# Optimization experiments

Hardware: AMD Instinct MI355X
Metric: run time of the kernel (lower is better)

## Reference

```python
import jax, jax.numpy as jnp
import numpy as np

EMBED = 1024
HEADS = 16
GQA_GROUPS = 2
KV_HEADS = HEADS // GQA_GROUPS  # 8
HEAD_DIM = EMBED // HEADS       # 64
ALIBI_ALPHA = 1.0
START_I = 0
N, S = 2, 2048


def setup_inputs() -> dict:
    key = jax.random.key(0)
    ks = jax.random.split(key, 6)
    x = jax.random.normal(ks[0], (N, S, EMBED), dtype=jnp.float32)
    sc = 1.0 / np.sqrt(EMBED)
    Wq = jax.random.normal(ks[1], (HEADS * HEAD_DIM, EMBED), dtype=jnp.float32) * sc
    Wk = jax.random.normal(ks[2], (KV_HEADS * HEAD_DIM, EMBED), dtype=jnp.float32) * sc
    Wv = jax.random.normal(ks[3], (KV_HEADS * HEAD_DIM, EMBED), dtype=jnp.float32) * sc
    Wo = jax.random.normal(ks[4], (EMBED, HEADS * HEAD_DIM), dtype=jnp.float32) * sc
    bo = jax.random.normal(ks[5], (EMBED,), dtype=jnp.float32) * 0.01
    return {"x": x, "Wq": Wq, "Wk": Wk, "Wv": Wv, "Wo": Wo, "bo": bo}


def _alibi_bias(q_len, k_len):
    # slopes[i] = 2**(-alpha*(i+start)) for i in 1..heads  -> shape (1,H,1,1)
    i = jnp.arange(1, HEADS + 1, dtype=jnp.float32)
    slopes = jnp.exp2(-ALIBI_ALPHA * (i + START_I)).reshape(1, HEADS, 1, 1)
    t_q = jnp.arange(q_len, dtype=jnp.float32)
    t_k = jnp.arange(k_len, dtype=jnp.float32)
    dist = jnp.abs(t_q[:, None] - t_k[None, :])  # (Q,K), symmetric (non-causal ALiBi)
    return -dist[None, None] * slopes            # (1,H,Q,K)


def reference(x, Wq, Wk, Wv, Wo, bo):
    n, s, _ = x.shape
    q = (x @ Wq.T).reshape(n, s, HEADS, HEAD_DIM)      # nqhd
    k = (x @ Wk.T).reshape(n, s, KV_HEADS, HEAD_DIM)   # nkhd (kv heads)
    v = (x @ Wv.T).reshape(n, s, KV_HEADS, HEAD_DIM)
    # GQA: repeat_interleave kv heads along head dim
    k = jnp.repeat(k, GQA_GROUPS, axis=2)
    v = jnp.repeat(v, GQA_GROUPS, axis=2)
    energy = jnp.einsum("nqhd,nkhd->nhqk", q, k)
    energy = energy + _alibi_bias(s, s)
    # NOTE: original divides (energy + bias) by sqrt(head_dim) inside softmax
    attn = jax.nn.softmax(energy / jnp.sqrt(jnp.float32(HEAD_DIM)), axis=-1)
    out = jnp.einsum("nhqk,nkhd->nqhd", attn, v).reshape(n, s, HEADS * HEAD_DIM)
    return out @ Wo.T + bo
```

## Files before the change

kernel.cpp:

```cpp
#include <hip/hip_runtime.h>

typedef _Float16 f16;
typedef f16 f16x8 __attribute__((ext_vector_type(8)));
typedef f16 f16x4 __attribute__((ext_vector_type(4)));
typedef float f32x4 __attribute__((ext_vector_type(4)));
typedef float f32x16 __attribute__((ext_vector_type(16)));
typedef unsigned uint4v __attribute__((ext_vector_type(4)));

#define GLL(g, l) __builtin_amdgcn_global_load_lds((const __attribute__((address_space(1))) void*)(g), (__attribute__((address_space(3))) void*)(l), 16, 0, 0)

__global__ __launch_bounds__(256) void cvt_all(
    const float* __restrict__ x, const float* __restrict__ wq, const float* __restrict__ wk,
    const float* __restrict__ wv, const float* __restrict__ wo,
    f16* __restrict__ xh, f16* __restrict__ wqh, f16* __restrict__ wkh,
    f16* __restrict__ wvh, f16* __restrict__ woh)
{
  int i = blockIdx.x * 256 + threadIdx.x;
  const float4* src; f16x4* dst; int off;
  if (i < 1048576)      { src = (const float4*)x;  dst = (f16x4*)xh;  off = i; }
  else if (i < 1310720) { src = (const float4*)wq; dst = (f16x4*)wqh; off = i - 1048576; }
  else if (i < 1441792) { src = (const float4*)wk; dst = (f16x4*)wkh; off = i - 1310720; }
  else if (i < 1572864) { src = (const float4*)wv; dst = (f16x4*)wvh; off = i - 1441792; }
  else                  { src = (const float4*)wo; dst = (f16x4*)woh; off = i - 1572864; }
  float4 v = src[off];
  f16x4 hv; hv[0] = (f16)v.x; hv[1] = (f16)v.y; hv[2] = (f16)v.z; hv[3] = (f16)v.w;
  dst[off] = hv;
}

template<int MODE>
__global__ __launch_bounds__(256) void gemm_k(
    const f16* __restrict__ A, const f16* __restrict__ B0, const f16* __restrict__ B1,
    const f16* __restrict__ B2,
    f16* __restrict__ Qb, f16* __restrict__ Kb, f16* __restrict__ VTb,
    const float* __restrict__ bo, float* __restrict__ Co)
{
  __shared__ __align__(16) f16 Ah[2][4096];
  __shared__ __align__(16) f16 Bh[2][4096];
  const int tid = threadIdx.x;
  const int bm = blockIdx.x & 31, bn = blockIdx.x >> 5;
  const f16* Bp;
  if (MODE == 0) {
    if (bn < 8)       Bp = B0 + (size_t)bn * 131072;
    else if (bn < 12) Bp = B1 + (size_t)(bn - 8) * 131072;
    else              Bp = B2 + (size_t)(bn - 12) * 131072;
  } else {
    Bp = B0 + (size_t)bn * 131072;
  }
  const f16* Ap = A + (size_t)bm * 131072;

  const int w = tid >> 6, lane = tid & 63, lr = lane & 15, lg = lane >> 4;
  const int wr = w >> 1, wc = w & 1;

  auto stage = [&](int b, int kt) {
#pragma unroll
    for (int i = 0; i < 2; ++i) {
      int o = tid * 16 + i * 4096;
      int row = o >> 6, colb = o & 63;
      GLL((const char*)Ap + (size_t)row * 2048 + kt * 64 + colb, (char*)&Ah[b][0] + o);
      GLL((const char*)Bp + (size_t)row * 2048 + kt * 64 + colb, (char*)&Bh[b][0] + o);
    }
  };

  f32x4 acc[4][4] = {};

  stage(0, 0);
  for (int kt = 0; kt < 32; ++kt) {
    const int cur = kt & 1;
    __syncthreads();
    if (kt < 31) stage(cur ^ 1, kt + 1);
    f16x8 af[4], bf[4];
#pragma unroll
    for (int mi = 0; mi < 4; ++mi)
      af[mi] = *(const f16x8*)((const char*)&Ah[cur][0] + (wr * 64 + mi * 16 + lr) * 64 + lg * 16);
#pragma unroll
    for (int ni = 0; ni < 4; ++ni)
      bf[ni] = *(const f16x8*)((const char*)&Bh[cur][0] + (wc * 64 + ni * 16 + lr) * 64 + lg * 16);
#pragma unroll
    for (int mi = 0; mi < 4; ++mi)
#pragma unroll
      for (int ni = 0; ni < 4; ++ni)
        acc[mi][ni] = __builtin_amdgcn_mfma_f32_16x16x32_f16(af[mi], bf[ni], acc[mi][ni], 0, 0, 0);
    __syncthreads();
  }

#pragma unroll
  for (int mi = 0; mi < 4; ++mi) {
#pragma unroll
    for (int ni = 0; ni < 4; ++ni) {
      const int ncol = bn * 128 + wc * 64 + ni * 16 + lr;
#pragma unroll
      for (int j = 0; j < 4; ++j) {
        const int m = bm * 128 + wr * 64 + mi * 16 + lg * 4 + j;
        const float v = acc[mi][ni][j];
        if (MODE == 0) {
          const int nb = m >> 11, s = m & 2047;
          if (ncol < 1024) {
            const int hh = ncol >> 6, d = ncol & 63;
            Qb[(((size_t)(nb * 16 + hh)) * 2048 + s) * 64 + d] = (f16)v;
          } else if (ncol < 1536) {
            const int kh = (ncol - 1024) >> 6, d = ncol & 63;
            Kb[(((size_t)(nb * 8 + kh)) * 2048 + s) * 64 + d] = (f16)v;
          } else {
            const int vh = (ncol - 1536) >> 6, d = ncol & 63;
            VTb[(((size_t)(nb * 8 + vh)) * 64 + d) * 2048 + s] = (f16)v;
          }
        } else {
          Co[(size_t)m * 1024 + ncol] = v + bo[ncol];
        }
      }
    }
  }
}

__global__ __launch_bounds__(256, 2) void attn_k(
    const f16* __restrict__ Qb, const f16* __restrict__ Kb, const f16* __restrict__ VTb,
    f16* __restrict__ Ob)
{
  __shared__ __align__(16) f16 KV[2][2][4096];

  const int tid = threadIdx.x, w = tid >> 6, l = tid & 63;
  const int lq = l & 31, hi = l >> 5;
  const int qt = blockIdx.x, nh = blockIdx.y;
  const int n = nh >> 4, h = nh & 15, kvh = h >> 1;
  const int qb = qt * 128;
  const int qhat = qb + w * 32 + lq;

  const f16* Qp = Qb + ((size_t)(n * 16 + h) * 2048 + qhat) * 64;
  f16x8 qf[4];
#pragma unroll
  for (int cd = 0; cd < 4; ++cd)
    qf[cd] = *(const f16x8*)(Qp + cd * 16 + hi * 8);

  const char* Kg = (const char*)(Kb + (size_t)(n * 8 + kvh) * 2048 * 64);
  const char* Vg = (const char*)(VTb + (size_t)(n * 8 + kvh) * 64 * 2048);

  const int s0 = tid * 16, s1 = tid * 16 + 4096;
  const int r0 = s0 >> 7, c0 = ((s0 >> 4) & 7) ^ (r0 & 7);
  const int r1 = s1 >> 7, c1 = ((s1 >> 4) & 7) ^ (r1 & 7);

  auto stageK = [&](int buf, int tb) {
    GLL(Kg + (size_t)(tb * 64 + r0) * 128 + c0 * 16, (char*)&KV[buf][0][0] + s0);
    GLL(Kg + (size_t)(tb * 64 + r1) * 128 + c1 * 16, (char*)&KV[buf][0][0] + s1);
  };
  auto stageV = [&](int buf, int tb) {
    GLL(Vg + (size_t)r0 * 4096 + tb * 128 + c0 * 16, (char*)&KV[buf][1][0] + s0);
    GLL(Vg + (size_t)r1 * 4096 + tb * 128 + c1 * 16, (char*)&KV[buf][1][0] + s1);
  };

  f32x16 oacc[2] = {};
  float p[2][16];
  float m_r = -1e30f, l_r = 0.f;
  const float C1 = 0.18033688011112042f;
  const float slt = exp2f(-(float)(h + 1)) * C1;
  const float qpos = (float)qhat;

  stageK(0, 0); stageV(0, 0);

  for (int t = 0; t < 32; ++t) {
    const int cur = t & 1;
    __syncthreads();
    if (t < 31) { stageK(cur ^ 1, t + 1); stageV(cur ^ 1, t + 1); }

#pragma unroll
    for (int kt = 0; kt < 2; ++kt) {
      f32x16 c = {};
#pragma unroll
      for (int cd = 0; cd < 4; ++cd) {
        const int row = kt * 32 + lq;
        f16x8 kf = *(const f16x8*)((const char*)&KV[cur][0][0] + row * 128 + (((2 * cd + hi) ^ (row & 7)) * 16));
        c = __builtin_amdgcn_mfma_f32_32x32x16_f16(kf, qf[cd], c, 0, 0, 0);
      }
      const float kb0 = (float)(t * 64 + kt * 32 + 4 * hi);
#pragma unroll
      for (int r = 0; r < 16; ++r) {
        float kpos = kb0 + (float)((r & 3) + 8 * (r >> 2));
        p[kt][r] = c[r] * C1 - fabsf(qpos - kpos) * slt;
      }
    }
    float pmax = p[0][0];
#pragma unroll
    for (int kt = 0; kt < 2; ++kt)
#pragma unroll
      for (int r = 0; r < 16; ++r) pmax = fmaxf(pmax, p[kt][r]);
    pmax = fmaxf(pmax, __shfl_xor(pmax, 32));

    if (!__all(pmax - m_r <= 8.0f)) {
      float mn = fmaxf(m_r, pmax);
      float sc = __builtin_amdgcn_exp2f(m_r - mn);
      m_r = mn; l_r *= sc;
#pragma unroll
      for (int dt = 0; dt < 2; ++dt)
#pragma unroll
        for (int r = 0; r < 16; ++r) oacc[dt][r] *= sc;
    }
    float ps = 0.f;
#pragma unroll
    for (int kt = 0; kt < 2; ++kt)
#pragma unroll
      for (int r = 0; r < 16; ++r) {
        float e = __builtin_amdgcn_exp2f(p[kt][r] - m_r);
        p[kt][r] = e; ps += e;
      }
    ps += __shfl_xor(ps, 32);
    l_r += ps;

    f16x8 pf[4];
#pragma unroll
    for (int c2 = 0; c2 < 4; ++c2) {
      const int T = c2 >> 1, e = c2 & 1;
      unsigned w0 = __builtin_bit_cast(unsigned, __builtin_amdgcn_cvt_pkrtz(p[T][8 * e + 0], p[T][8 * e + 1]));
      unsigned w2 = __builtin_bit_cast(unsigned, __builtin_amdgcn_cvt_pkrtz(p[T][8 * e + 4], p[T][8 * e + 5]));
      unsigned w1 = __builtin_bit_cast(unsigned, __builtin_amdgcn_cvt_pkrtz(p[T][8 * e + 2], p[T][8 * e + 3]));
      unsigned w3 = __builtin_bit_cast(unsigned, __builtin_amdgcn_cvt_pkrtz(p[T][8 * e + 6], p[T][8 * e + 7]));
      asm volatile("v_permlane32_swap_b32 %0, %1" : "+v"(w0), "+v"(w2));
      asm volatile("v_permlane32_swap_b32 %0, %1" : "+v"(w1), "+v"(w3));
      uint4v pu; pu.x = w0; pu.y = w1; pu.z = w2; pu.w = w3;
      pf[c2] = __builtin_bit_cast(f16x8, pu);
    }

#pragma unroll
    for (int dt = 0; dt < 2; ++dt) {
#pragma unroll
      for (int ck = 0; ck < 4; ++ck) {
        const int row = dt * 32 + lq;
        f16x8 vf = *(const f16x8*)((const char*)&KV[cur][1][0] + row * 128 + (((2 * ck + hi) ^ (row & 7)) * 16));
        oacc[dt] = __builtin_amdgcn_mfma_f32_32x32x16_f16(vf, pf[ck], oacc[dt], 0, 0, 0);
      }
    }
  }

  __syncthreads();
  f16* Ot = (f16*)&KV[0][0][0];
  const float invl = 1.0f / l_r;
#pragma unroll
  for (int dt = 0; dt < 2; ++dt)
#pragma unroll
    for (int r = 0; r < 16; ++r) {
      const int d = dt * 32 + (r & 3) + 8 * (r >> 2) + 4 * hi;
      Ot[(w * 32 + lq) * 72 + d] = (f16)(oacc[dt][r] * invl);
    }
  __syncthreads();
  {
    const int q = tid >> 1, hf = tid & 1;
    const f16* src = &Ot[q * 72 + hf * 32];
    f16* dst = Ob + (size_t)(n * 2048 + qb + q) * 1024 + h * 64 + hf * 32;
#pragma unroll
    for (int i = 0; i < 4; ++i)
      *(f16x8*)(dst + i * 8) = *(const f16x8*)(src + i * 8);
  }
}

extern "C" void kernel_launch(void* const* d_in, const int* in_sizes, int n_in,
                              void* d_out, int out_size, void* d_ws, size_t ws_size,
                              hipStream_t stream) {
  const float* x  = (const float*)d_in[0];
  const float* Wq = (const float*)d_in[1];
  const float* Wk = (const float*)d_in[2];
  const float* Wv = (const float*)d_in[3];
  const float* Wo = (const float*)d_in[4];
  const float* bo = (const float*)d_in[5];

  char* ws = (char*)d_ws;
  f16* xh  = (f16*)(ws);
  f16* wqh = (f16*)(ws + 8388608);
  f16* wkh = (f16*)(ws + 10485760);
  f16* wvh = (f16*)(ws + 11534336);
  f16* woh = (f16*)(ws + 12582912);
  f16* Qb  = (f16*)(ws + 14680064);
  f16* Kb  = (f16*)(ws + 23068672);
  f16* VTb = (f16*)(ws + 27262976);
  f16* Ob  = (f16*)(ws + 31457280);

  cvt_all<<<7168, 256, 0, stream>>>(x, Wq, Wk, Wv, Wo, xh, wqh, wkh, wvh, woh);
  gemm_k<0><<<512, 256, 0, stream>>>(xh, wqh, wkh, wvh, Qb, Kb, VTb, nullptr, nullptr);
  attn_k<<<dim3(16, 32), 256, 0, stream>>>(Qb, Kb, VTb, Ob);
  gemm_k<1><<<256, 256, 0, stream>>>(Ob, woh, nullptr, nullptr, nullptr, nullptr, nullptr, bo, (float*)d_out);
}
```

Measured before the change: 139.4 us.

## Split attention KV range across two wave groups per block and merge

The attention block grows from 256 to 512 threads. Each half of the waves processes half of the key/value sequence for the same 128 queries, using its own double-buffered LDS region. At the end the partial softmax states (m, l, O) are merged through shared memory before the normalized output is written. This doubles the waves working per query tile, raising occupancy and latency hiding on a grid of only 512 blocks. The cost is extra LDS use (64KB per block), additional barriers, and a merge epilogue.

```diff
diff --git a/kernel.cpp b/kernel.cpp
--- a/kernel.cpp
+++ b/kernel.cpp
@@ -112,18 +112,19 @@
   }
 }
 
-__global__ __launch_bounds__(256, 2) void attn_k(
+__global__ __launch_bounds__(512, 4) void attn_k(
     const f16* __restrict__ Qb, const f16* __restrict__ Kb, const f16* __restrict__ VTb,
     f16* __restrict__ Ob)
 {
-  __shared__ __align__(16) f16 KV[2][2][4096];
+  __shared__ __align__(16) char SMEM[65536];
 
   const int tid = threadIdx.x, w = tid >> 6, l = tid & 63;
   const int lq = l & 31, hi = l >> 5;
+  const int half = w >> 2, g = w & 3;
   const int qt = blockIdx.x, nh = blockIdx.y;
   const int n = nh >> 4, h = nh & 15, kvh = h >> 1;
   const int qb = qt * 128;
-  const int qhat = qb + w * 32 + lq;
+  const int qhat = qb + g * 32 + lq;
 
   const f16* Qp = Qb + ((size_t)(n * 16 + h) * 2048 + qhat) * 64;
   f16x8 qf[4];
@@ -134,17 +135,21 @@
   const char* Kg = (const char*)(Kb + (size_t)(n * 8 + kvh) * 2048 * 64);
   const char* Vg = (const char*)(VTb + (size_t)(n * 8 + kvh) * 64 * 2048);
 
-  const int s0 = tid * 16, s1 = tid * 16 + 4096;
+  const int t256 = tid & 255;
+  const int s0 = t256 * 16, s1 = s0 + 4096;
   const int r0 = s0 >> 7, c0 = ((s0 >> 4) & 7) ^ (r0 & 7);
   const int r1 = s1 >> 7, c1 = ((s1 >> 4) & 7) ^ (r1 & 7);
+  char* KB0 = SMEM + half * 32768;
 
   auto stageK = [&](int buf, int tb) {
-    GLL(Kg + (size_t)(tb * 64 + r0) * 128 + c0 * 16, (char*)&KV[buf][0][0] + s0);
-    GLL(Kg + (size_t)(tb * 64 + r1) * 128 + c1 * 16, (char*)&KV[buf][0][0] + s1);
+    char* d = KB0 + buf * 16384;
+    GLL(Kg + (size_t)(tb * 64 + r0) * 128 + c0 * 16, d + s0);
+    GLL(Kg + (size_t)(tb * 64 + r1) * 128 + c1 * 16, d + s1);
   };
   auto stageV = [&](int buf, int tb) {
-    GLL(Vg + (size_t)r0 * 4096 + tb * 128 + c0 * 16, (char*)&KV[buf][1][0] + s0);
-    GLL(Vg + (size_t)r1 * 4096 + tb * 128 + c1 * 16, (char*)&KV[buf][1][0] + s1);
+    char* d = KB0 + buf * 16384 + 8192;
+    GLL(Vg + (size_t)r0 * 4096 + tb * 128 + c0 * 16, d + s0);
+    GLL(Vg + (size_t)r1 * 4096 + tb * 128 + c1 * 16, d + s1);
   };
 
   f32x16 oacc[2] = {};
@@ -154,12 +159,15 @@
   const float slt = exp2f(-(float)(h + 1)) * C1;
   const float qpos = (float)qhat;
 
-  stageK(0, 0); stageV(0, 0);
-
-  for (int t = 0; t < 32; ++t) {
+  stageK(0, half * 16); stageV(0, half * 16);
+
+  for (int t = 0; t < 16; ++t) {
     const int cur = t & 1;
+    const int tb = half * 16 + t;
     __syncthreads();
-    if (t < 31) { stageK(cur ^ 1, t + 1); stageV(cur ^ 1, t + 1); }
+    if (t < 15) { stageK(cur ^ 1, tb + 1); stageV(cur ^ 1, tb + 1); }
+    const char* Kl = KB0 + cur * 16384;
+    const char* Vl = Kl + 8192;
 
 #pragma unroll
     for (int kt = 0; kt < 2; ++kt) {
@@ -167,10 +175,10 @@
 #pragma unroll
       for (int cd = 0; cd < 4; ++cd) {
         const int row = kt * 32 + lq;
-        f16x8 kf = *(const f16x8*)((const char*)&KV[cur][0][0] + row * 128 + (((2 * cd + hi) ^ (row & 7)) * 16));
+        f16x8 kf = *(const f16x8*)(Kl + row * 128 + (((2 * cd + hi) ^ (row & 7)) * 16));
         c = __builtin_amdgcn_mfma_f32_32x32x16_f16(kf, qf[cd], c, 0, 0, 0);
       }
-      const float kb0 = (float)(t * 64 + kt * 32 + 4 * hi);
+      const float kb0 = (float)(tb * 64 + kt * 32 + 4 * hi);
 #pragma unroll
       for (int r = 0; r < 16; ++r) {
         float kpos = kb0 + (float)((r & 3) + 8 * (r >> 2));
@@ -223,30 +231,61 @@
 #pragma unroll
       for (int ck = 0; ck < 4; ++ck) {
         const int row = dt * 32 + lq;
-        f16x8 vf = *(const f16x8*)((const char*)&KV[cur][1][0] + row * 128 + (((2 * ck + hi) ^ (row & 7)) * 16));
+        f16x8 vf = *(const f16x8*)(Vl + row * 128 + (((2 * ck + hi) ^ (row & 7)) * 16));
         oacc[dt] = __builtin_amdgcn_mfma_f32_32x32x16_f16(vf, pf[ck], oacc[dt], 0, 0, 0);
       }
     }
   }
 
+  float* Xo = (float*)SMEM;
+  float* Xm = (float*)(SMEM + 33792);
+  float* Xl = (float*)(SMEM + 34304);
+  f16* Ot = (f16*)SMEM;
+
   __syncthreads();
-  f16* Ot = (f16*)&KV[0][0][0];
-  const float invl = 1.0f / l_r;
-#pragma unroll
-  for (int dt = 0; dt < 2; ++dt)
-#pragma unroll
-    for (int r = 0; r < 16; ++r) {
-      const int d = dt * 32 + (r & 3) + 8 * (r >> 2) + 4 * hi;
-      Ot[(w * 32 + lq) * 72 + d] = (f16)(oacc[dt][r] * invl);
-    }
+  if (half) {
+#pragma unroll
+    for (int dt = 0; dt < 2; ++dt)
+#pragma unroll
+      for (int r = 0; r < 16; ++r) {
+        const int d = dt * 32 + (r & 3) + 8 * (r >> 2) + 4 * hi;
+        Xo[(g * 32 + lq) * 66 + d] = oacc[dt][r];
+      }
+    if (!hi) { Xm[g * 32 + lq] = m_r; Xl[g * 32 + lq] = l_r; }
+  }
+  __syncthreads();
+  float fin[2][16];
+  if (!half) {
+    const float m1 = Xm[g * 32 + lq], l1 = Xl[g * 32 + lq];
+    const float mm = fmaxf(m_r, m1);
+    const float a0 = __builtin_amdgcn_exp2f(m_r - mm);
+    const float a1 = __builtin_amdgcn_exp2f(m1 - mm);
+    const float linv = 1.0f / (l_r * a0 + l1 * a1);
+#pragma unroll
+    for (int dt = 0; dt < 2; ++dt)
+#pragma unroll
+      for (int r = 0; r < 16; ++r) {
+        const int d = dt * 32 + (r & 3) + 8 * (r >> 2) + 4 * hi;
+        fin[dt][r] = (oacc[dt][r] * a0 + Xo[(g * 32 + lq) * 66 + d] * a1) * linv;
+      }
+  }
+  __syncthreads();
+  if (!half) {
+#pragma unroll
+    for (int dt = 0; dt < 2; ++dt)
+#pragma unroll
+      for (int r = 0; r < 16; ++r) {
+        const int d = dt * 32 + (r & 3) + 8 * (r >> 2) + 4 * hi;
+        Ot[(g * 32 + lq) * 72 + d] = (f16)fin[dt][r];
+      }
+  }
   __syncthreads();
   {
-    const int q = tid >> 1, hf = tid & 1;
-    const f16* src = &Ot[q * 72 + hf * 32];
-    f16* dst = Ob + (size_t)(n * 2048 + qb + q) * 1024 + h * 64 + hf * 32;
-#pragma unroll
-    for (int i = 0; i < 4; ++i)
-      *(f16x8*)(dst + i * 8) = *(const f16x8*)(src + i * 8);
+    const int q = tid >> 2, seg = tid & 3;
+    const f16* src = &Ot[q * 72 + seg * 16];
+    f16* dst = Ob + (size_t)(n * 2048 + qb + q) * 1024 + h * 64 + seg * 16;
+    *(f16x8*)(dst) = *(const f16x8*)(src);
+    *(f16x8*)(dst + 8) = *(const f16x8*)(src + 8);
   }
 }
 
@@ -273,6 +312,6 @@
 
   cvt_all<<<7168, 256, 0, stream>>>(x, Wq, Wk, Wv, Wo, xh, wqh, wkh, wvh, woh);
   gemm_k<0><<<512, 256, 0, stream>>>(xh, wqh, wkh, wvh, Qb, Kb, VTb, nullptr, nullptr);
-  attn_k<<<dim3(16, 32), 256, 0, stream>>>(Qb, Kb, VTb, Ob);
+  attn_k<<<dim3(16, 32), 512, 0, stream>>>(Qb, Kb, VTb, Ob);
   gemm_k<1><<<256, 256, 0, stream>>>(Ob, woh, nullptr, nullptr, nullptr, nullptr, nullptr, bo, (float*)d_out);
 }
```

New measurement: 133.4 us. 1.04x faster.
